# Performance work log

Hardware: AMD Instinct MI355X
Metric: run time of the kernel (lower is better)

The kernel has to match this reference:

```python
import jax, jax.numpy as jnp
import numpy as np
import math

HEAD_DIM = 64
HEAD_NUM = 8  # hidden_dim(512) // head_dim(64)
EPS = 1e-8


def modulated_linear(x, s, weight, aff_w, aff_b):
    # x: [B, N, IN], s: [B, S], weight: [OUT, IN], aff_w: [IN, S], aff_b: [IN]
    style = s @ aff_w.T + aff_b                       # [B, IN]
    w = weight[None, :, :] * style[:, None, :]        # [B, OUT, IN]
    demod = jax.lax.rsqrt(jnp.sum(w * w, axis=2) + EPS)  # [B, OUT]
    w = w * demod[:, :, None]
    return jnp.einsum('bni,boi->bno', x, w)           # [B, N, OUT]


def setup_inputs() -> dict:
    key = jax.random.key(0)
    ks = jax.random.split(key, 8)
    B, N, F, S = 8, 1024, 512, 512
    sc = 1.0 / math.sqrt(F)
    return {
        'x': jax.random.normal(ks[0], (B, N, F), dtype=jnp.float32),
        's': jax.random.normal(ks[1], (B, S), dtype=jnp.float32),
        'k_weight': jax.random.normal(ks[2], (F, F), dtype=jnp.float32) * sc,
        'k_aff_w': jax.random.normal(ks[3], (F, S), dtype=jnp.float32) * sc,
        'k_aff_b': jnp.ones((F,), dtype=jnp.float32),
        'o_weight': jax.random.normal(ks[4], (F, F), dtype=jnp.float32) * sc,
        'o_aff_w': jax.random.normal(ks[5], (F, S), dtype=jnp.float32) * sc,
        'o_aff_b': jnp.ones((F,), dtype=jnp.float32),
    }


def reference(x, s, k_weight, k_aff_w, k_aff_b, o_weight, o_aff_w, o_aff_b):
    B, N, _ = x.shape
    # Original code computes q, k, v all via k_mapping (faithful to the bug).
    kqv = modulated_linear(x, s, k_weight, k_aff_w, k_aff_b)  # [B, N, hidden]
    kqv = kqv.reshape(B, N, HEAD_NUM, HEAD_DIM)               # [B, N, H, D]
    q = k = v = kqv
    scale = 1.0 / math.sqrt(HEAD_DIM)
    scores = jnp.einsum('bnhd,bmhd->bhnm', q, k) * scale      # [B, H, N, N]
    attn = jax.nn.softmax(scores, axis=-1)
    out = jnp.einsum('bhnm,bmhd->bnhd', attn, v)              # [B, N, H, D]
    out = out.reshape(B, N, HEAD_NUM * HEAD_DIM)
    return modulated_linear(out, s, o_weight, o_aff_w, o_aff_b)
```

## Files before the change

kernel.cpp:

```cpp
#include <hip/hip_runtime.h>
#include <stdint.h>

using short8  = __attribute__((ext_vector_type(8))) short;
using f32x4   = __attribute__((ext_vector_type(4))) float;
using float4v = __attribute__((ext_vector_type(4))) float;
using u16x4   = __attribute__((ext_vector_type(4))) unsigned short;

__device__ __forceinline__ unsigned short f2b(float f) {
    union { float f; unsigned int i; } v; v.f = f;
    unsigned int i = v.i;
    unsigned int r = (i + 0x7fffu + ((i >> 16) & 1u)) >> 16;
    return (unsigned short)r;
}
__device__ __forceinline__ unsigned short f2bt(float f) {
    union { float f; unsigned int i; } v; v.f = f;
    return (unsigned short)(v.i >> 16);
}
__device__ __forceinline__ short8 ld8(const unsigned short* p) {
    return *reinterpret_cast<const short8*>(p);
}
__device__ __forceinline__ void st8(unsigned short* p, short8 v) {
    *reinterpret_cast<short8*>(p) = v;
}
__device__ __forceinline__ f32x4 mfma16(short8 a, short8 b, f32x4 c) {
    return __builtin_amdgcn_mfma_f32_16x16x32_bf16(a, b, c, 0, 0, 0);
}
__device__ __forceinline__ void stC(float* p, float v)          { *p = v; }
__device__ __forceinline__ void stC(unsigned short* p, float v) { *p = f2b(v); }

__global__ __launch_bounds__(256) void cvt_kernel(const float* __restrict__ in,
                                                  unsigned short* __restrict__ out)
{
    int i = blockIdx.x * 256 + threadIdx.x;
    float4v v = reinterpret_cast<const float4v*>(in)[i];
    u16x4 o;
#pragma unroll
    for (int j = 0; j < 4; ++j) o[j] = f2b(v[j]);
    reinterpret_cast<u16x4*>(out)[i] = o;
}

__global__ __launch_bounds__(256) void style_kernel(
    const float* __restrict__ s,
    const float* __restrict__ k_aff_w, const float* __restrict__ k_aff_b,
    const float* __restrict__ o_aff_w, const float* __restrict__ o_aff_b,
    float* __restrict__ style)
{
    int wid  = blockIdx.x * 4 + (threadIdx.x >> 6);
    int lane = threadIdx.x & 63;
    int map  = wid >> 12;
    int rem  = wid & 4095;
    int b    = rem >> 9;
    int i    = rem & 511;
    const float* aw = map ? o_aff_w : k_aff_w;
    const float* ab = map ? o_aff_b : k_aff_b;
    const float* sp = s  + b * 512 + lane * 8;
    const float* wp = aw + i * 512 + lane * 8;
    float acc = 0.f;
#pragma unroll
    for (int j = 0; j < 8; ++j) acc += sp[j] * wp[j];
#pragma unroll
    for (int off = 1; off < 64; off <<= 1) acc += __shfl_xor(acc, off, 64);
    if (lane == 0) style[(map * 8 + b) * 512 + i] = acc + ab[i];
}

__global__ __launch_bounds__(256) void modw_kernel(
    const float* __restrict__ k_weight,
    const float* __restrict__ o_weight,
    const float* __restrict__ style,
    unsigned short* __restrict__ wmod)
{
    int wid  = blockIdx.x * 4 + (threadIdx.x >> 6);
    int lane = threadIdx.x & 63;
    int map  = wid >> 12;
    int rem  = wid & 4095;
    int b    = rem >> 9;
    int o    = rem & 511;
    const float* wrow = (map ? o_weight : k_weight) + o * 512 + lane * 8;
    const float* st   = style + (map * 8 + b) * 512 + lane * 8;
    float w[8]; float ss = 0.f;
#pragma unroll
    for (int j = 0; j < 8; ++j) { w[j] = wrow[j] * st[j]; ss += w[j] * w[j]; }
#pragma unroll
    for (int off = 1; off < 64; off <<= 1) ss += __shfl_xor(ss, off, 64);
    float demod = rsqrtf(ss + 1e-8f);
    short8 ov;
#pragma unroll
    for (int j = 0; j < 8; ++j) ov[j] = (short)f2b(w[j] * demod);
    unsigned short* dst = wmod + (((size_t)map * 8 + b) * 512 + o) * 512 + lane * 8;
    *reinterpret_cast<short8*>(dst) = ov;
}

template <typename CT>
__global__ __launch_bounds__(256) void gemm_bt_lds_kernel(
    const unsigned short* __restrict__ A,
    const unsigned short* __restrict__ Bt,
    CT* __restrict__ C)
{
    constexpr int KP = 40;
    int blk = blockIdx.x;
    int nt = blk & 7;
    int mt = (blk >> 3) & 7;
    int b  = blk >> 6;
    int tid  = threadIdx.x;
    int w    = tid >> 6;
    int lane = tid & 63;
    int quad = lane >> 4;
    int r    = lane & 15;
    int wm   = w >> 1;
    int wn   = w & 1;

    __shared__ __align__(16) unsigned short As[2][128][KP];
    __shared__ __align__(16) unsigned short Bs[2][64][KP];

    const unsigned short* Ab = A  + ((size_t)b * 1024 + mt * 128) * 512;
    const unsigned short* Bb = Bt + ((size_t)b * 512  + nt * 64 ) * 512;

    int srow = lane >> 2;
    int scol = (lane & 3) * 8;
    const unsigned short* ga0 = Ab + (size_t)(w * 32 + srow) * 512 + scol;
    const unsigned short* ga1 = ga0 + (size_t)16 * 512;
    const unsigned short* gb0 = Bb + (size_t)(w * 16 + srow) * 512 + scol;

    f32x4 acc[4][2];
#pragma unroll
    for (int i = 0; i < 4; ++i)
#pragma unroll
        for (int j = 0; j < 2; ++j) acc[i][j] = f32x4{0.f, 0.f, 0.f, 0.f};

    {
        short8 pa0 = ld8(ga0), pa1 = ld8(ga1), pb0 = ld8(gb0);
        st8(&As[0][w * 32 + srow][scol],      pa0);
        st8(&As[0][w * 32 + 16 + srow][scol], pa1);
        st8(&Bs[0][w * 16 + srow][scol],      pb0);
    }
    __syncthreads();

    for (int ks = 0; ks < 16; ++ks) {
        int s = ks & 1;
        short8 pa0, pa1, pb0;
        if (ks < 15) {
            int ko = (ks + 1) * 32;
            pa0 = ld8(ga0 + ko);
            pa1 = ld8(ga1 + ko);
            pb0 = ld8(gb0 + ko);
        }
        short8 af[4], bf[2];
#pragma unroll
        for (int i = 0; i < 4; ++i)
            af[i] = ld8(&As[s][wm * 64 + i * 16 + r][quad * 8]);
#pragma unroll
        for (int j = 0; j < 2; ++j)
            bf[j] = ld8(&Bs[s][wn * 32 + j * 16 + r][quad * 8]);
#pragma unroll
        for (int i = 0; i < 4; ++i)
#pragma unroll
            for (int j = 0; j < 2; ++j)
                acc[i][j] = mfma16(af[i], bf[j], acc[i][j]);
        if (ks < 15) {
            int ns = s ^ 1;
            st8(&As[ns][w * 32 + srow][scol],      pa0);
            st8(&As[ns][w * 32 + 16 + srow][scol], pa1);
            st8(&Bs[ns][w * 16 + srow][scol],      pb0);
        }
        __syncthreads();
    }

    CT* Cb = C + (size_t)b * 1024 * 512;
#pragma unroll
    for (int i = 0; i < 4; ++i) {
#pragma unroll
        for (int rr = 0; rr < 4; ++rr) {
            int row = mt * 128 + wm * 64 + i * 16 + quad * 4 + rr;
#pragma unroll
            for (int j = 0; j < 2; ++j) {
                int col = nt * 64 + wn * 32 + j * 16 + r;
                stC(Cb + (size_t)row * 512 + col, acc[i][j][rr]);
            }
        }
    }
}

__global__ void transpose_kernel(const unsigned short* __restrict__ kqv,
                                 unsigned short* __restrict__ vt)
{
    __shared__ unsigned short tile[32][33];
    int bh = blockIdx.x;
    int b  = bh >> 3, h = bh & 7;
    int d0 = blockIdx.y * 32;
    int n0 = blockIdx.z * 32;
    int tx = threadIdx.x;
    int ty = threadIdx.y;
    const unsigned short* src = kqv + (size_t)b * 1024 * 512 + h * 64;
#pragma unroll
    for (int i = 0; i < 32; i += 8)
        tile[ty + i][tx] = src[(size_t)(n0 + ty + i) * 512 + d0 + tx];
    __syncthreads();
    unsigned short* dst = vt + ((size_t)bh * 64 + d0) * 1024 + n0;
#pragma unroll
    for (int i = 0; i < 32; i += 8)
        dst[(size_t)(ty + i) * 1024 + tx] = tile[tx][ty + i];
}

__global__ __launch_bounds__(256) void attn_kernel(
    const unsigned short* __restrict__ kqv,
    const unsigned short* __restrict__ vt,
    unsigned short* __restrict__ attn_out)
{
    constexpr int PAD = 72;
    int blk = blockIdx.x;
    int bh = blk & 63;
    int qt = blk >> 6;
    int b  = bh >> 3, h = bh & 7;
    int tid  = threadIdx.x;
    int wv   = tid >> 6;
    int lane = tid & 63;
    int quad = lane >> 4;
    int r    = lane & 15;

    __shared__ __align__(16) unsigned short klds[2][64][PAD];
    __shared__ __align__(16) unsigned short vlds[2][64][PAD];
    __shared__ __align__(16) unsigned short plds[4][16][PAD];
    unsigned short* myp = &plds[wv][0][0];

    const unsigned short* Mb = kqv + (size_t)b * 1024 * 512;
    int q0 = qt * 64 + wv * 16;

    const unsigned short* qptr = Mb + (size_t)(q0 + r) * 512 + h * 64 + quad * 8;
    short8 bq0 = ld8(qptr);
    short8 bq1 = ld8(qptr + 32);

    short8 ones;
#pragma unroll
    for (int j = 0; j < 8; ++j) ones[j] = (short)0x3F80;

    f32x4 o0 = {0.f, 0.f, 0.f, 0.f};
    f32x4 o1 = o0, o2 = o0, o3 = o0, lacc = o0;

    int srow0 = tid >> 3;
    int srow1 = srow0 + 32;
    int scol  = (tid & 7) * 8;
    const unsigned short* Kg = Mb + h * 64;
    const unsigned short* Vg = vt + (size_t)bh * 64 * 1024;

    {
        short8 k0v = ld8(Kg + (size_t)srow0 * 512 + scol);
        short8 k1v = ld8(Kg + (size_t)srow1 * 512 + scol);
        short8 v0v = ld8(Vg + (size_t)srow0 * 1024 + scol);
        short8 v1v = ld8(Vg + (size_t)srow1 * 1024 + scol);
        st8(&klds[0][srow0][scol], k0v);
        st8(&klds[0][srow1][scol], k1v);
        st8(&vlds[0][srow0][scol], v0v);
        st8(&vlds[0][srow1][scol], v1v);
    }
    __syncthreads();

    const float c  = 0.18033688011112042f;
    const float CM = 28.853900817779268f;

    for (int it = 0; it < 16; ++it) {
        int s = it & 1;
        short8 pk0, pk1, pv0, pv1;
        if (it < 15) {
            int k0n = (it + 1) * 64;
            pk0 = ld8(Kg + (size_t)(k0n + srow0) * 512 + scol);
            pk1 = ld8(Kg + (size_t)(k0n + srow1) * 512 + scol);
            pv0 = ld8(Vg + (size_t)srow0 * 1024 + k0n + scol);
            pv1 = ld8(Vg + (size_t)srow1 * 1024 + k0n + scol);
        }
        f32x4 st_[4];
#pragma unroll
        for (int t = 0; t < 4; ++t) {
            short8 ka = ld8(&klds[s][t * 16 + r][quad * 8]);
            short8 kb = ld8(&klds[s][t * 16 + r][32 + quad * 8]);
            f32x4 sacc = {0.f, 0.f, 0.f, 0.f};
            sacc = mfma16(ka, bq0, sacc);
            sacc = mfma16(kb, bq1, sacc);
            st_[t] = sacc;
        }
#pragma unroll
        for (int t = 0; t < 4; ++t) {
            u16x4 pb;
#pragma unroll
            for (int rr = 0; rr < 4; ++rr)
                pb[rr] = f2bt(exp2f(st_[t][rr] * c - CM));
            *reinterpret_cast<u16x4*>(&myp[r * PAD + t * 16 + quad * 4]) = pb;
        }
        short8 ap0 = ld8(&myp[r * PAD + quad * 8]);
        short8 ap1 = ld8(&myp[r * PAD + 32 + quad * 8]);
        {
            short8 va, vb;
            va = ld8(&vlds[s][0 * 16 + r][quad * 8]);
            vb = ld8(&vlds[s][0 * 16 + r][32 + quad * 8]);
            o0 = mfma16(ap0, va, o0);  o0 = mfma16(ap1, vb, o0);
            va = ld8(&vlds[s][1 * 16 + r][quad * 8]);
            vb = ld8(&vlds[s][1 * 16 + r][32 + quad * 8]);
            o1 = mfma16(ap0, va, o1);  o1 = mfma16(ap1, vb, o1);
            va = ld8(&vlds[s][2 * 16 + r][quad * 8]);
            vb = ld8(&vlds[s][2 * 16 + r][32 + quad * 8]);
            o2 = mfma16(ap0, va, o2);  o2 = mfma16(ap1, vb, o2);
            va = ld8(&vlds[s][3 * 16 + r][quad * 8]);
            vb = ld8(&vlds[s][3 * 16 + r][32 + quad * 8]);
            o3 = mfma16(ap0, va, o3);  o3 = mfma16(ap1, vb, o3);
            lacc = mfma16(ap0, ones, lacc);
            lacc = mfma16(ap1, ones, lacc);
        }
        if (it < 15) {
            int ns = s ^ 1;
            st8(&klds[ns][srow0][scol], pk0);
            st8(&klds[ns][srow1][scol], pk1);
            st8(&vlds[ns][srow0][scol], pv0);
            st8(&vlds[ns][srow1][scol], pv1);
        }
        __syncthreads();
    }

    unsigned short* ob = attn_out + (size_t)b * 1024 * 512 + (size_t)h * 64;
#pragma unroll
    for (int rr = 0; rr < 4; ++rr) {
        float inv = 1.0f / lacc[rr];
        int n = q0 + quad * 4 + rr;
        unsigned short* orow = ob + (size_t)n * 512 + r;
        orow[0]  = f2b(o0[rr] * inv);
        orow[16] = f2b(o1[rr] * inv);
        orow[32] = f2b(o2[rr] * inv);
        orow[48] = f2b(o3[rr] * inv);
    }
}

extern "C" void kernel_launch(void* const* d_in, const int* in_sizes, int n_in,
                              void* d_out, int out_size, void* d_ws, size_t ws_size,
                              hipStream_t stream)
{
    const float* x        = (const float*)d_in[0];
    const float* s        = (const float*)d_in[1];
    const float* k_weight = (const float*)d_in[2];
    const float* k_aff_w  = (const float*)d_in[3];
    const float* k_aff_b  = (const float*)d_in[4];
    const float* o_weight = (const float*)d_in[5];
    const float* o_aff_w  = (const float*)d_in[6];
    const float* o_aff_b  = (const float*)d_in[7];
    float* out = (float*)d_out;

    char* ws = (char*)d_ws;
    float* style          = (float*)ws;
    unsigned short* wmod  = (unsigned short*)(ws + 32 * 1024);
    unsigned short* xbf   = wmod + (size_t)2 * 8 * 512 * 512;
    unsigned short* kqv   = xbf  + (size_t)8 * 1024 * 512;
    unsigned short* vt    = kqv  + (size_t)8 * 1024 * 512;
    unsigned short* attn  = xbf;

    cvt_kernel<<<4096, 256, 0, stream>>>(x, xbf);
    style_kernel<<<2048, 256, 0, stream>>>(s, k_aff_w, k_aff_b, o_aff_w, o_aff_b, style);
    modw_kernel<<<2048, 256, 0, stream>>>(k_weight, o_weight, style, wmod);
    gemm_bt_lds_kernel<unsigned short><<<512, 256, 0, stream>>>(xbf, wmod, kqv);
    transpose_kernel<<<dim3(64, 2, 32), dim3(32, 8), 0, stream>>>(kqv, vt);
    attn_kernel<<<1024, 256, 0, stream>>>(kqv, vt, attn);
    gemm_bt_lds_kernel<float><<<512, 256, 0, stream>>>(attn, wmod + (size_t)8 * 512 * 512, out);
}
```

Baseline: 167.4 us.

## Fuse V transpose into GEMM epilogue and process two query tiles per attention wave

Drops the separate transpose kernel. The first GEMM now writes a transposed bf16 copy of its output tile through LDS into the vt buffer. The attention kernel gives each wave 32 queries (two 16-row groups), halving the grid, so each K/V tile loaded into LDS is reused for twice as many queries. LDS padding also changes. The cost is more registers, fewer blocks (512) available to hide latency, and extra LDS traffic in the GEMM epilogue.

```diff
diff --git a/kernel.cpp b/kernel.cpp
--- a/kernel.cpp
+++ b/kernel.cpp
@@ -90,13 +90,21 @@
     *reinterpret_cast<short8*>(dst) = ov;
 }
 
-template <typename CT>
+template <typename CT, bool WVT>
 __global__ __launch_bounds__(256) void gemm_bt_lds_kernel(
     const unsigned short* __restrict__ A,
     const unsigned short* __restrict__ Bt,
-    CT* __restrict__ C)
+    CT* __restrict__ C,
+    unsigned short* __restrict__ VT)
 {
     constexpr int KP = 40;
+    constexpr int TP = 136;
+    __shared__ __align__(16) unsigned short smem[2 * 128 * KP + 2 * 64 * KP];
+    typedef unsigned short APlane[128][KP];
+    typedef unsigned short BPlane[64][KP];
+    APlane* As = reinterpret_cast<APlane*>(smem);
+    BPlane* Bs = reinterpret_cast<BPlane*>(smem + 2 * 128 * KP);
+
     int blk = blockIdx.x;
     int nt = blk & 7;
     int mt = (blk >> 3) & 7;
@@ -109,9 +117,6 @@
     int wm   = w >> 1;
     int wn   = w & 1;
 
-    __shared__ __align__(16) unsigned short As[2][128][KP];
-    __shared__ __align__(16) unsigned short Bs[2][64][KP];
-
     const unsigned short* Ab = A  + ((size_t)b * 1024 + mt * 128) * 512;
     const unsigned short* Bb = Bt + ((size_t)b * 512  + nt * 64 ) * 512;
 
@@ -166,6 +171,7 @@
     }
 
     CT* Cb = C + (size_t)b * 1024 * 512;
+    unsigned short (*Tt)[TP] = reinterpret_cast<unsigned short (*)[TP]>(smem);
 #pragma unroll
     for (int i = 0; i < 4; ++i) {
 #pragma unroll
@@ -177,28 +183,32 @@
                 stC(Cb + (size_t)row * 512 + col, acc[i][j][rr]);
             }
         }
-    }
-}
-
-__global__ void transpose_kernel(const unsigned short* __restrict__ kqv,
-                                 unsigned short* __restrict__ vt)
-{
-    __shared__ unsigned short tile[32][33];
-    int bh = blockIdx.x;
-    int b  = bh >> 3, h = bh & 7;
-    int d0 = blockIdx.y * 32;
-    int n0 = blockIdx.z * 32;
-    int tx = threadIdx.x;
-    int ty = threadIdx.y;
-    const unsigned short* src = kqv + (size_t)b * 1024 * 512 + h * 64;
-#pragma unroll
-    for (int i = 0; i < 32; i += 8)
-        tile[ty + i][tx] = src[(size_t)(n0 + ty + i) * 512 + d0 + tx];
-    __syncthreads();
-    unsigned short* dst = vt + ((size_t)bh * 64 + d0) * 1024 + n0;
-#pragma unroll
-    for (int i = 0; i < 32; i += 8)
-        dst[(size_t)(ty + i) * 1024 + tx] = tile[tx][ty + i];
+        if (WVT) {
+#pragma unroll
+            for (int j = 0; j < 2; ++j) {
+                int d = wn * 32 + j * 16 + r;
+#pragma unroll
+                for (int rh = 0; rh < 2; ++rh) {
+                    int row = wm * 64 + i * 16 + quad * 4 + rh * 2;
+                    unsigned int pv = (unsigned int)f2b(acc[i][j][rh * 2]) |
+                                      ((unsigned int)f2b(acc[i][j][rh * 2 + 1]) << 16);
+                    *reinterpret_cast<unsigned int*>(&Tt[d][row]) = pv;
+                }
+            }
+        }
+    }
+    if (WVT) {
+        __syncthreads();
+        int d  = tid >> 2;
+        int cc = tid & 3;
+        const unsigned short* src = &Tt[d][cc * 32];
+        unsigned short* dst = VT + ((size_t)(b * 8 + nt) * 64 + d) * 1024 + mt * 128 + cc * 32;
+        short8 t0 = ld8(src), t1 = ld8(src + 8), t2 = ld8(src + 16), t3 = ld8(src + 24);
+        st8(dst,      t0);
+        st8(dst + 8,  t1);
+        st8(dst + 16, t2);
+        st8(dst + 24, t3);
+    }
 }
 
 __global__ __launch_bounds__(256) void attn_kernel(
@@ -206,7 +216,7 @@
     const unsigned short* __restrict__ vt,
     unsigned short* __restrict__ attn_out)
 {
-    constexpr int PAD = 72;
+    constexpr int PAD = 68;
     int blk = blockIdx.x;
     int bh = blk & 63;
     int qt = blk >> 6;
@@ -219,22 +229,31 @@
 
     __shared__ __align__(16) unsigned short klds[2][64][PAD];
     __shared__ __align__(16) unsigned short vlds[2][64][PAD];
-    __shared__ __align__(16) unsigned short plds[4][16][PAD];
-    unsigned short* myp = &plds[wv][0][0];
+    __shared__ __align__(16) unsigned short plds[4][2][16][PAD];
+    unsigned short (*myp)[16][PAD] = plds[wv];
 
     const unsigned short* Mb = kqv + (size_t)b * 1024 * 512;
-    int q0 = qt * 64 + wv * 16;
-
-    const unsigned short* qptr = Mb + (size_t)(q0 + r) * 512 + h * 64 + quad * 8;
-    short8 bq0 = ld8(qptr);
-    short8 bq1 = ld8(qptr + 32);
+    int q0 = qt * 128 + wv * 32;
+
+    short8 bq[2][2];
+#pragma unroll
+    for (int g = 0; g < 2; ++g) {
+        const unsigned short* qp = Mb + (size_t)(q0 + g * 16 + r) * 512 + h * 64 + quad * 8;
+        bq[g][0] = ld8(qp);
+        bq[g][1] = ld8(qp + 32);
+    }
 
     short8 ones;
 #pragma unroll
     for (int j = 0; j < 8; ++j) ones[j] = (short)0x3F80;
 
-    f32x4 o0 = {0.f, 0.f, 0.f, 0.f};
-    f32x4 o1 = o0, o2 = o0, o3 = o0, lacc = o0;
+    f32x4 o[2][4], lacc[2];
+#pragma unroll
+    for (int g = 0; g < 2; ++g) {
+        lacc[g] = f32x4{0.f, 0.f, 0.f, 0.f};
+#pragma unroll
+        for (int j = 0; j < 4; ++j) o[g][j] = f32x4{0.f, 0.f, 0.f, 0.f};
+    }
 
     int srow0 = tid >> 3;
     int srow1 = srow0 + 32;
@@ -267,42 +286,49 @@
             pv0 = ld8(Vg + (size_t)srow0 * 1024 + k0n + scol);
             pv1 = ld8(Vg + (size_t)srow1 * 1024 + k0n + scol);
         }
-        f32x4 st_[4];
+        f32x4 st_[2][4];
 #pragma unroll
         for (int t = 0; t < 4; ++t) {
             short8 ka = ld8(&klds[s][t * 16 + r][quad * 8]);
             short8 kb = ld8(&klds[s][t * 16 + r][32 + quad * 8]);
-            f32x4 sacc = {0.f, 0.f, 0.f, 0.f};
-            sacc = mfma16(ka, bq0, sacc);
-            sacc = mfma16(kb, bq1, sacc);
-            st_[t] = sacc;
+#pragma unroll
+            for (int g = 0; g < 2; ++g) {
+                f32x4 sacc = {0.f, 0.f, 0.f, 0.f};
+                sacc = mfma16(ka, bq[g][0], sacc);
+                sacc = mfma16(kb, bq[g][1], sacc);
+                st_[g][t] = sacc;
+            }
+        }
+#pragma unroll
+        for (int g = 0; g < 2; ++g)
+#pragma unroll
+            for (int t = 0; t < 4; ++t) {
+                u16x4 pb;
+#pragma unroll
+                for (int rr = 0; rr < 4; ++rr)
+                    pb[rr] = f2bt(exp2f(st_[g][t][rr] * c - CM));
+                *reinterpret_cast<u16x4*>(&myp[g][r][t * 16 + quad * 4]) = pb;
+            }
+        short8 ap[2][2];
+#pragma unroll
+        for (int g = 0; g < 2; ++g) {
+            ap[g][0] = ld8(&myp[g][r][quad * 8]);
+            ap[g][1] = ld8(&myp[g][r][32 + quad * 8]);
         }
 #pragma unroll
         for (int t = 0; t < 4; ++t) {
-            u16x4 pb;
-#pragma unroll
-            for (int rr = 0; rr < 4; ++rr)
-                pb[rr] = f2bt(exp2f(st_[t][rr] * c - CM));
-            *reinterpret_cast<u16x4*>(&myp[r * PAD + t * 16 + quad * 4]) = pb;
-        }
-        short8 ap0 = ld8(&myp[r * PAD + quad * 8]);
-        short8 ap1 = ld8(&myp[r * PAD + 32 + quad * 8]);
-        {
-            short8 va, vb;
-            va = ld8(&vlds[s][0 * 16 + r][quad * 8]);
-            vb = ld8(&vlds[s][0 * 16 + r][32 + quad * 8]);
-            o0 = mfma16(ap0, va, o0);  o0 = mfma16(ap1, vb, o0);
-            va = ld8(&vlds[s][1 * 16 + r][quad * 8]);
-            vb = ld8(&vlds[s][1 * 16 + r][32 + quad * 8]);
-            o1 = mfma16(ap0, va, o1);  o1 = mfma16(ap1, vb, o1);
-            va = ld8(&vlds[s][2 * 16 + r][quad * 8]);
-            vb = ld8(&vlds[s][2 * 16 + r][32 + quad * 8]);
-            o2 = mfma16(ap0, va, o2);  o2 = mfma16(ap1, vb, o2);
-            va = ld8(&vlds[s][3 * 16 + r][quad * 8]);
-            vb = ld8(&vlds[s][3 * 16 + r][32 + quad * 8]);
-            o3 = mfma16(ap0, va, o3);  o3 = mfma16(ap1, vb, o3);
-            lacc = mfma16(ap0, ones, lacc);
-            lacc = mfma16(ap1, ones, lacc);
+            short8 va = ld8(&vlds[s][t * 16 + r][quad * 8]);
+            short8 vb = ld8(&vlds[s][t * 16 + r][32 + quad * 8]);
+#pragma unroll
+            for (int g = 0; g < 2; ++g) {
+                o[g][t] = mfma16(ap[g][0], va, o[g][t]);
+                o[g][t] = mfma16(ap[g][1], vb, o[g][t]);
+            }
+        }
+#pragma unroll
+        for (int g = 0; g < 2; ++g) {
+            lacc[g] = mfma16(ap[g][0], ones, lacc[g]);
+            lacc[g] = mfma16(ap[g][1], ones, lacc[g]);
         }
         if (it < 15) {
             int ns = s ^ 1;
@@ -316,15 +342,17 @@
 
     unsigned short* ob = attn_out + (size_t)b * 1024 * 512 + (size_t)h * 64;
 #pragma unroll
-    for (int rr = 0; rr < 4; ++rr) {
-        float inv = 1.0f / lacc[rr];
-        int n = q0 + quad * 4 + rr;
-        unsigned short* orow = ob + (size_t)n * 512 + r;
-        orow[0]  = f2b(o0[rr] * inv);
-        orow[16] = f2b(o1[rr] * inv);
-        orow[32] = f2b(o2[rr] * inv);
-        orow[48] = f2b(o3[rr] * inv);
-    }
+    for (int g = 0; g < 2; ++g)
+#pragma unroll
+        for (int rr = 0; rr < 4; ++rr) {
+            float inv = 1.0f / lacc[g][rr];
+            int n = q0 + g * 16 + quad * 4 + rr;
+            unsigned short* orow = ob + (size_t)n * 512 + r;
+            orow[0]  = f2b(o[g][0][rr] * inv);
+            orow[16] = f2b(o[g][1][rr] * inv);
+            orow[32] = f2b(o[g][2][rr] * inv);
+            orow[48] = f2b(o[g][3][rr] * inv);
+        }
 }
 
 extern "C" void kernel_launch(void* const* d_in, const int* in_sizes, int n_in,
@@ -352,8 +380,7 @@
     cvt_kernel<<<4096, 256, 0, stream>>>(x, xbf);
     style_kernel<<<2048, 256, 0, stream>>>(s, k_aff_w, k_aff_b, o_aff_w, o_aff_b, style);
     modw_kernel<<<2048, 256, 0, stream>>>(k_weight, o_weight, style, wmod);
-    gemm_bt_lds_kernel<unsigned short><<<512, 256, 0, stream>>>(xbf, wmod, kqv);
-    transpose_kernel<<<dim3(64, 2, 32), dim3(32, 8), 0, stream>>>(kqv, vt);
-    attn_kernel<<<1024, 256, 0, stream>>>(kqv, vt, attn);
-    gemm_bt_lds_kernel<float><<<512, 256, 0, stream>>>(attn, wmod + (size_t)8 * 512 * 512, out);
-}
+    gemm_bt_lds_kernel<unsigned short, true><<<512, 256, 0, stream>>>(xbf, wmod, kqv, vt);
+    attn_kernel<<<512, 256, 0, stream>>>(kqv, vt, attn);
+    gemm_bt_lds_kernel<float, false><<<512, 256, 0, stream>>>(attn, wmod + (size_t)8 * 512 * 512, out, nullptr);
+}
```

After: 209.7 us. 1.25x slower.

## Fuse V transpose into GEMM epilogue and use async global-to-LDS loads

Applied to the files above, without the earlier changes.

The first GEMM now writes a transposed bf16 copy of its output tile through shared memory straight to the V^T buffer, so the separate transpose kernel and its extra read of kqv are gone. The GEMM mainloop switches from register-staged loads to global_load_lds direct copies into unpadded LDS (KP 40 to 32). The attention kernel's LDS padding also changes from 72 to 68. Unpadded LDS may add bank conflicts on fragment reads. There is no explicit wait on the async copies beyond __syncthreads, so ordering relies on the compiler inserting one.

```diff
diff --git a/kernel.cpp b/kernel.cpp
--- a/kernel.cpp
+++ b/kernel.cpp
@@ -27,6 +27,13 @@
 }
 __device__ __forceinline__ void stC(float* p, float v)          { *p = v; }
 __device__ __forceinline__ void stC(unsigned short* p, float v) { *p = f2b(v); }
+
+__device__ __forceinline__ void async_cp16(const unsigned short* g, unsigned short* l) {
+    __builtin_amdgcn_global_load_lds(
+        (const __attribute__((address_space(1))) unsigned int*)(const void*)g,
+        (__attribute__((address_space(3))) unsigned int*)(void*)l,
+        16, 0, 0);
+}
 
 __global__ __launch_bounds__(256) void cvt_kernel(const float* __restrict__ in,
                                                   unsigned short* __restrict__ out)
@@ -90,13 +97,21 @@
     *reinterpret_cast<short8*>(dst) = ov;
 }
 
-template <typename CT>
+template <typename CT, bool WVT>
 __global__ __launch_bounds__(256) void gemm_bt_lds_kernel(
     const unsigned short* __restrict__ A,
     const unsigned short* __restrict__ Bt,
-    CT* __restrict__ C)
-{
-    constexpr int KP = 40;
+    CT* __restrict__ C,
+    unsigned short* __restrict__ VT)
+{
+    constexpr int KP = 32;
+    constexpr int TP = 136;
+    __shared__ __align__(16) unsigned short smem[2 * 128 * KP + 2 * 64 * KP];
+    typedef unsigned short APlane[128][KP];
+    typedef unsigned short BPlane[64][KP];
+    APlane* As = reinterpret_cast<APlane*>(smem);
+    BPlane* Bs = reinterpret_cast<BPlane*>(smem + 2 * 128 * KP);
+
     int blk = blockIdx.x;
     int nt = blk & 7;
     int mt = (blk >> 3) & 7;
@@ -109,9 +124,6 @@
     int wm   = w >> 1;
     int wn   = w & 1;
 
-    __shared__ __align__(16) unsigned short As[2][128][KP];
-    __shared__ __align__(16) unsigned short Bs[2][64][KP];
-
     const unsigned short* Ab = A  + ((size_t)b * 1024 + mt * 128) * 512;
     const unsigned short* Bb = Bt + ((size_t)b * 512  + nt * 64 ) * 512;
 
@@ -127,22 +139,19 @@
 #pragma unroll
         for (int j = 0; j < 2; ++j) acc[i][j] = f32x4{0.f, 0.f, 0.f, 0.f};
 
-    {
-        short8 pa0 = ld8(ga0), pa1 = ld8(ga1), pb0 = ld8(gb0);
-        st8(&As[0][w * 32 + srow][scol],      pa0);
-        st8(&As[0][w * 32 + 16 + srow][scol], pa1);
-        st8(&Bs[0][w * 16 + srow][scol],      pb0);
-    }
+    async_cp16(ga0, &As[0][w * 32][0]);
+    async_cp16(ga1, &As[0][w * 32 + 16][0]);
+    async_cp16(gb0, &Bs[0][w * 16][0]);
     __syncthreads();
 
     for (int ks = 0; ks < 16; ++ks) {
         int s = ks & 1;
-        short8 pa0, pa1, pb0;
         if (ks < 15) {
+            int ns = s ^ 1;
             int ko = (ks + 1) * 32;
-            pa0 = ld8(ga0 + ko);
-            pa1 = ld8(ga1 + ko);
-            pb0 = ld8(gb0 + ko);
+            async_cp16(ga0 + ko, &As[ns][w * 32][0]);
+            async_cp16(ga1 + ko, &As[ns][w * 32 + 16][0]);
+            async_cp16(gb0 + ko, &Bs[ns][w * 16][0]);
         }
         short8 af[4], bf[2];
 #pragma unroll
@@ -156,16 +165,11 @@
 #pragma unroll
             for (int j = 0; j < 2; ++j)
                 acc[i][j] = mfma16(af[i], bf[j], acc[i][j]);
-        if (ks < 15) {
-            int ns = s ^ 1;
-            st8(&As[ns][w * 32 + srow][scol],      pa0);
-            st8(&As[ns][w * 32 + 16 + srow][scol], pa1);
-            st8(&Bs[ns][w * 16 + srow][scol],      pb0);
-        }
         __syncthreads();
     }
 
     CT* Cb = C + (size_t)b * 1024 * 512;
+    unsigned short (*Tt)[TP] = reinterpret_cast<unsigned short (*)[TP]>(smem);
 #pragma unroll
     for (int i = 0; i < 4; ++i) {
 #pragma unroll
@@ -177,28 +181,32 @@
                 stC(Cb + (size_t)row * 512 + col, acc[i][j][rr]);
             }
         }
-    }
-}
-
-__global__ void transpose_kernel(const unsigned short* __restrict__ kqv,
-                                 unsigned short* __restrict__ vt)
-{
-    __shared__ unsigned short tile[32][33];
-    int bh = blockIdx.x;
-    int b  = bh >> 3, h = bh & 7;
-    int d0 = blockIdx.y * 32;
-    int n0 = blockIdx.z * 32;
-    int tx = threadIdx.x;
-    int ty = threadIdx.y;
-    const unsigned short* src = kqv + (size_t)b * 1024 * 512 + h * 64;
-#pragma unroll
-    for (int i = 0; i < 32; i += 8)
-        tile[ty + i][tx] = src[(size_t)(n0 + ty + i) * 512 + d0 + tx];
-    __syncthreads();
-    unsigned short* dst = vt + ((size_t)bh * 64 + d0) * 1024 + n0;
-#pragma unroll
-    for (int i = 0; i < 32; i += 8)
-        dst[(size_t)(ty + i) * 1024 + tx] = tile[tx][ty + i];
+        if (WVT) {
+#pragma unroll
+            for (int j = 0; j < 2; ++j) {
+                int d = wn * 32 + j * 16 + r;
+#pragma unroll
+                for (int rh = 0; rh < 2; ++rh) {
+                    int row = wm * 64 + i * 16 + quad * 4 + rh * 2;
+                    unsigned int pv = (unsigned int)f2b(acc[i][j][rh * 2]) |
+                                      ((unsigned int)f2b(acc[i][j][rh * 2 + 1]) << 16);
+                    *reinterpret_cast<unsigned int*>(&Tt[d][row]) = pv;
+                }
+            }
+        }
+    }
+    if (WVT) {
+        __syncthreads();
+        int d  = tid >> 2;
+        int cc = tid & 3;
+        const unsigned short* src = &Tt[d][cc * 32];
+        unsigned short* dst = VT + ((size_t)(b * 8 + nt) * 64 + d) * 1024 + mt * 128 + cc * 32;
+        short8 t0 = ld8(src), t1 = ld8(src + 8), t2 = ld8(src + 16), t3 = ld8(src + 24);
+        st8(dst,      t0);
+        st8(dst + 8,  t1);
+        st8(dst + 16, t2);
+        st8(dst + 24, t3);
+    }
 }
 
 __global__ __launch_bounds__(256) void attn_kernel(
@@ -206,7 +214,7 @@
     const unsigned short* __restrict__ vt,
     unsigned short* __restrict__ attn_out)
 {
-    constexpr int PAD = 72;
+    constexpr int PAD = 68;
     int blk = blockIdx.x;
     int bh = blk & 63;
     int qt = blk >> 6;
@@ -352,8 +360,7 @@
     cvt_kernel<<<4096, 256, 0, stream>>>(x, xbf);
     style_kernel<<<2048, 256, 0, stream>>>(s, k_aff_w, k_aff_b, o_aff_w, o_aff_b, style);
     modw_kernel<<<2048, 256, 0, stream>>>(k_weight, o_weight, style, wmod);
-    gemm_bt_lds_kernel<unsigned short><<<512, 256, 0, stream>>>(xbf, wmod, kqv);
-    transpose_kernel<<<dim3(64, 2, 32), dim3(32, 8), 0, stream>>>(kqv, vt);
+    gemm_bt_lds_kernel<unsigned short, true><<<512, 256, 0, stream>>>(xbf, wmod, kqv, vt);
     attn_kernel<<<1024, 256, 0, stream>>>(kqv, vt, attn);
-    gemm_bt_lds_kernel<float><<<512, 256, 0, stream>>>(attn, wmod + (size_t)8 * 512 * 512, out);
-}
+    gemm_bt_lds_kernel<float, false><<<512, 256, 0, stream>>>(attn, wmod + (size_t)8 * 512 * 512, out, nullptr);
+}
```

Measured after the change: 266.7 us. +59.3%, slower.
